# Kernel optimization log

Hardware: AMD Instinct MI355X
Metric: run time of the kernel (lower is better)

Reference implementation:

```python
import jax, jax.numpy as jnp
import numpy as np

B, K, N = 8, 4, 131072
T = B * K * N  # upper bound on packed length
NEG_IDLE = -1e8   # logit value forced when slot is idle
NEG_FILL = -1000.0  # padded-output fill value for logits


def setup_inputs() -> dict:
    key = jax.random.key(0)
    k1, k2, k3, k4, k5, k6 = jax.random.split(key, 6)
    return {
        "rgb": jax.random.normal(k1, (T, 3), dtype=jnp.float32),
        "logits_surface": jax.random.normal(k2, (T, 1), dtype=jnp.float32),
        "logits_air": jax.random.normal(k3, (T, 1), dtype=jnp.float32),
        "mask_surface": jax.random.bernoulli(k4, 0.5, (B, K, N)),
        "mask_air": jax.random.bernoulli(k5, 0.5, (B, K, N)),
        "idle_states": jax.random.uniform(k6, (B, K), dtype=jnp.float32),
    }


def reference(rgb, logits_surface, logits_air, mask_surface, mask_air, idle_states):
    # Packed arrays are laid out in flattened (b, k, n) order: the packed index of a
    # masked element equals the count of True entries preceding it -> cumsum - 1.
    Bb, Kk, Nn = mask_surface.shape
    scale = (1.0 - idle_states)[:, :, None, None]          # [B,K,1,1]
    idle = idle_states[:, :, None, None]                   # [B,K,1,1]

    ms_flat = mask_surface.reshape(-1)
    idx_s = (jnp.cumsum(ms_flat.astype(jnp.int32)) - 1).reshape(Bb, Kk, Nn)
    ms = mask_surface[..., None]                           # [B,K,N,1]

    rgb_g = jnp.take(rgb, idx_s, axis=0)                   # [B,K,N,3]
    rgb_out = jnp.where(ms, rgb_g * scale, 0.0)

    ls_g = jnp.take(logits_surface, idx_s, axis=0)         # [B,K,N,1]
    logits_surface_out = jnp.where(ms, ls_g * scale + idle * NEG_IDLE, NEG_FILL)

    ma_flat = mask_air.reshape(-1)
    idx_a = (jnp.cumsum(ma_flat.astype(jnp.int32)) - 1).reshape(Bb, Kk, Nn)
    ma = mask_air[..., None]
    la_g = jnp.take(logits_air, idx_a, axis=0)             # [B,K,N,1]
    logits_air_out = jnp.where(ma, la_g * scale + idle * NEG_IDLE, NEG_FILL)

    return rgb_out, logits_surface_out, logits_air_out
```

## Files before the change

### kernel.cpp

```cpp
#include <hip/hip_runtime.h>
#include <stdint.h>

#define T_TOTAL  4194304
#define NEG_IDLE (-100000000.0f)
#define NEG_FILL (-1000.0f)

#define BLOCK   256
#define EPT     8
#define EPB     (BLOCK * EPT)
#define NBLOCKS (T_TOTAL / EPB)


__device__ __forceinline__ unsigned decode8_i32(const uint4* p) {
    const uint4 a = p[0], b = p[1];
    return (a.x ? 1u : 0u) | (a.y ? 2u : 0u) | (a.z ? 4u : 0u) | (a.w ? 8u : 0u)
         | (b.x ? 16u : 0u) | (b.y ? 32u : 0u) | (b.z ? 64u : 0u) | (b.w ? 128u : 0u);
}

__global__ __launch_bounds__(BLOCK) void reduce_pack_kernel(
    const uint4* __restrict__ ms,
    const uint4* __restrict__ ma,
    unsigned long long* __restrict__ sums,
    unsigned short* __restrict__ packed)
{
    const int blk  = blockIdx.x;
    const int tid  = threadIdx.x;
    const int lane = tid & 63;
    const int wave = tid >> 6;
    const size_t e = (size_t)blk * EPB + (size_t)tid * EPT;

    const unsigned bits_s = decode8_i32(ms + (e >> 2));
    const unsigned bits_a = decode8_i32(ma + (e >> 2));
    packed[blk * BLOCK + tid] = (unsigned short)(bits_s | (bits_a << 8));

    unsigned long long v =
        ((unsigned long long)(unsigned)__popc(bits_a) << 32) | (unsigned)__popc(bits_s);
    #pragma unroll
    for (int d = 32; d; d >>= 1) v += __shfl_down(v, d, 64);

    __shared__ unsigned long long w[BLOCK / 64];
    if (lane == 0) w[wave] = v;
    __syncthreads();
    if (tid == 0) sums[blk] = w[0] + w[1] + w[2] + w[3];
}

__global__ __launch_bounds__(BLOCK) void scatter_kernel(
    const float* __restrict__ rgb,
    const float* __restrict__ ls,
    const float* __restrict__ la,
    const unsigned long long* __restrict__ sums,
    const unsigned short* __restrict__ packed,
    const float* __restrict__ idle_states,
    float* __restrict__ out)
{
    const int blk  = blockIdx.x;
    const int tid  = threadIdx.x;
    const int lane = tid & 63;
    const int wave = tid >> 6;
    const size_t base = (size_t)blk * EPB + (size_t)tid * EPT;

    const unsigned p = packed[blk * BLOCK + tid];
    const unsigned bits_s = p & 0xffu;
    const unsigned bits_a = p >> 8;

    unsigned long long acc = 0;
    {
        const ulonglong2* s2 = (const ulonglong2*)sums;
        const int i0 = tid * 8;
        #pragma unroll
        for (int q = 0; q < 4; ++q) {
            const ulonglong2 v = s2[tid * 4 + q];
            const int i = i0 + 2 * q;
            acc += (i     < blk) ? v.x : 0ull;
            acc += (i + 1 < blk) ? v.y : 0ull;
        }
        #pragma unroll
        for (int d = 32; d; d >>= 1) acc += __shfl_down(acc, d, 64);
    }

    const unsigned long long pk =
        ((unsigned long long)(unsigned)__popc(bits_a) << 32) | (unsigned)__popc(bits_s);
    unsigned long long incl = pk;
    #pragma unroll
    for (int d = 1; d < 64; d <<= 1) {
        unsigned long long t = __shfl_up(incl, d, 64);
        if (lane >= d) incl += t;
    }
    unsigned long long excl = incl - pk;

    __shared__ unsigned long long wtot[BLOCK / 64];
    __shared__ unsigned long long wpre[BLOCK / 64];
    if (lane == 63) wtot[wave] = incl;
    if (lane == 0)  wpre[wave] = acc;
    __syncthreads();
    #pragma unroll
    for (int w = 0; w < BLOCK / 64; ++w)
        if (w < wave) excl += wtot[w];
    const unsigned long long pre = wpre[0] + wpre[1] + wpre[2] + wpre[3];

    const int idx_s0 = (int)((pre + excl) & 0xffffffffULL);
    const int idx_a0 = (int)((pre + excl) >> 32);

    int is_[EPT], ia_[EPT];
    #pragma unroll
    for (int j = 0; j < EPT; ++j) {
        is_[j] = idx_s0 + __popc(bits_s & ((1u << j) - 1u));
        ia_[j] = idx_a0 + __popc(bits_a & ((1u << j) - 1u));
    }

    float r[3 * EPT], sv[EPT], av[EPT];
    #pragma unroll
    for (int j = 0; j < EPT; ++j) {
        const float* rp = rgb + (size_t)is_[j] * 3;
        r[3 * j + 0] = rp[0];
        r[3 * j + 1] = rp[1];
        r[3 * j + 2] = rp[2];
        sv[j] = ls[is_[j]];
        av[j] = la[ia_[j]];
    }

    const float idle      = idle_states[blk >> 6];
    const float scale     = 1.0f - idle;
    const float idle_term = idle * NEG_IDLE;
    #pragma unroll
    for (int j = 0; j < EPT; ++j) {
        const bool bs = (bits_s >> j) & 1u;
        const bool ba = (bits_a >> j) & 1u;
        r[3 * j + 0] = bs ? r[3 * j + 0] * scale : 0.0f;
        r[3 * j + 1] = bs ? r[3 * j + 1] * scale : 0.0f;
        r[3 * j + 2] = bs ? r[3 * j + 2] * scale : 0.0f;
        sv[j] = bs ? (sv[j] * scale + idle_term) : NEG_FILL;
        av[j] = ba ? (av[j] * scale + idle_term) : NEG_FILL;
    }

    float4* prgb = (float4*)(out + base * 3);
    #pragma unroll
    for (int j = 0; j < 6; ++j) prgb[j] = ((const float4*)r)[j];

    float4* pls = (float4*)(out + (size_t)3 * T_TOTAL + base);
    pls[0] = ((const float4*)sv)[0];
    pls[1] = ((const float4*)sv)[1];

    float4* pla = (float4*)(out + (size_t)4 * T_TOTAL + base);
    pla[0] = ((const float4*)av)[0];
    pla[1] = ((const float4*)av)[1];
}

extern "C" void kernel_launch(void* const* d_in, const int* in_sizes, int n_in,
                              void* d_out, int out_size, void* d_ws, size_t ws_size,
                              hipStream_t stream) {
    const float* rgb  = (const float*)d_in[0];
    const float* ls   = (const float*)d_in[1];
    const float* la   = (const float*)d_in[2];
    const uint4* ms   = (const uint4*)d_in[3];
    const uint4* ma   = (const uint4*)d_in[4];
    const float* idle = (const float*)d_in[5];
    float* out = (float*)d_out;

    unsigned long long* sums   = (unsigned long long*)d_ws;
    unsigned short*     packed = (unsigned short*)((uint8_t*)d_ws + NBLOCKS * sizeof(unsigned long long));

    reduce_pack_kernel<<<NBLOCKS, BLOCK, 0, stream>>>(ms, ma, sums, packed);
    scatter_kernel<<<NBLOCKS, BLOCK, 0, stream>>>(rgb, ls, la, sums, packed,
                                                  idle, out);
}
```

Baseline: 185.3 us.

## Split scatter kernel into three output roles and use nontemporal loads/stores

Measured after the change: 232.0 us. 1.25x slower.

```diff
diff --git a/kernel.cpp b/kernel.cpp
--- a/kernel.cpp
+++ b/kernel.cpp
@@ -5,21 +5,25 @@
 #define NEG_IDLE (-100000000.0f)
 #define NEG_FILL (-1000.0f)
 
-#define BLOCK   256
-#define EPT     8
-#define EPB     (BLOCK * EPT)
-#define NBLOCKS (T_TOTAL / EPB)
+#define BLOCK  256
+#define EPT    8
+#define EPB    (BLOCK * EPT)
+#define NCHUNK (T_TOTAL / EPB)
 
 
-__device__ __forceinline__ unsigned decode8_i32(const uint4* p) {
-    const uint4 a = p[0], b = p[1];
+typedef float    f32x4 __attribute__((ext_vector_type(4)));
+typedef unsigned u32x4 __attribute__((ext_vector_type(4)));
+
+__device__ __forceinline__ unsigned decode8_i32(const u32x4* p) {
+    const u32x4 a = __builtin_nontemporal_load(p);
+    const u32x4 b = __builtin_nontemporal_load(p + 1);
     return (a.x ? 1u : 0u) | (a.y ? 2u : 0u) | (a.z ? 4u : 0u) | (a.w ? 8u : 0u)
          | (b.x ? 16u : 0u) | (b.y ? 32u : 0u) | (b.z ? 64u : 0u) | (b.w ? 128u : 0u);
 }
 
 __global__ __launch_bounds__(BLOCK) void reduce_pack_kernel(
-    const uint4* __restrict__ ms,
-    const uint4* __restrict__ ma,
+    const u32x4* __restrict__ ms,
+    const u32x4* __restrict__ ma,
     unsigned long long* __restrict__ sums,
     unsigned short* __restrict__ packed)
 {
@@ -53,15 +57,17 @@
     const float* __restrict__ idle_states,
     float* __restrict__ out)
 {
-    const int blk  = blockIdx.x;
+    const int bid  = blockIdx.x;
+    const int role = bid >> 11;
+    const int blk  = bid & (NCHUNK - 1);
     const int tid  = threadIdx.x;
     const int lane = tid & 63;
     const int wave = tid >> 6;
     const size_t base = (size_t)blk * EPB + (size_t)tid * EPT;
 
-    const unsigned p = packed[blk * BLOCK + tid];
-    const unsigned bits_s = p & 0xffu;
-    const unsigned bits_a = p >> 8;
+    const unsigned pw   = packed[blk * BLOCK + tid];
+    const unsigned bits = (role == 2) ? (pw >> 8) : (pw & 0xffu);
+    const int c = __popc(bits);
 
     unsigned long long acc = 0;
     {
@@ -78,17 +84,15 @@
         for (int d = 32; d; d >>= 1) acc += __shfl_down(acc, d, 64);
     }
 
-    const unsigned long long pk =
-        ((unsigned long long)(unsigned)__popc(bits_a) << 32) | (unsigned)__popc(bits_s);
-    unsigned long long incl = pk;
+    int incl = c;
     #pragma unroll
     for (int d = 1; d < 64; d <<= 1) {
-        unsigned long long t = __shfl_up(incl, d, 64);
+        const int t = __shfl_up(incl, d, 64);
         if (lane >= d) incl += t;
     }
-    unsigned long long excl = incl - pk;
+    int excl = incl - c;
 
-    __shared__ unsigned long long wtot[BLOCK / 64];
+    __shared__ int wtot[BLOCK / 64];
     __shared__ unsigned long long wpre[BLOCK / 64];
     if (lane == 63) wtot[wave] = incl;
     if (lane == 0)  wpre[wave] = acc;
@@ -97,53 +101,56 @@
     for (int w = 0; w < BLOCK / 64; ++w)
         if (w < wave) excl += wtot[w];
     const unsigned long long pre = wpre[0] + wpre[1] + wpre[2] + wpre[3];
+    const int pre32 = (role == 2) ? (int)(pre >> 32) : (int)(pre & 0xffffffffull);
+    const int idx0  = pre32 + excl;
 
-    const int idx_s0 = (int)((pre + excl) & 0xffffffffULL);
-    const int idx_a0 = (int)((pre + excl) >> 32);
-
-    int is_[EPT], ia_[EPT];
+    int idx[EPT];
     #pragma unroll
-    for (int j = 0; j < EPT; ++j) {
-        is_[j] = idx_s0 + __popc(bits_s & ((1u << j) - 1u));
-        ia_[j] = idx_a0 + __popc(bits_a & ((1u << j) - 1u));
-    }
-
-    float r[3 * EPT], sv[EPT], av[EPT];
-    #pragma unroll
-    for (int j = 0; j < EPT; ++j) {
-        const float* rp = rgb + (size_t)is_[j] * 3;
-        r[3 * j + 0] = rp[0];
-        r[3 * j + 1] = rp[1];
-        r[3 * j + 2] = rp[2];
-        sv[j] = ls[is_[j]];
-        av[j] = la[ia_[j]];
-    }
+    for (int j = 0; j < EPT; ++j)
+        idx[j] = idx0 + __popc(bits & ((1u << j) - 1u));
 
     const float idle      = idle_states[blk >> 6];
     const float scale     = 1.0f - idle;
     const float idle_term = idle * NEG_IDLE;
-    #pragma unroll
-    for (int j = 0; j < EPT; ++j) {
-        const bool bs = (bits_s >> j) & 1u;
-        const bool ba = (bits_a >> j) & 1u;
-        r[3 * j + 0] = bs ? r[3 * j + 0] * scale : 0.0f;
-        r[3 * j + 1] = bs ? r[3 * j + 1] * scale : 0.0f;
-        r[3 * j + 2] = bs ? r[3 * j + 2] * scale : 0.0f;
-        sv[j] = bs ? (sv[j] * scale + idle_term) : NEG_FILL;
-        av[j] = ba ? (av[j] * scale + idle_term) : NEG_FILL;
+
+    if (role == 0) {
+        float r[3 * EPT];
+        #pragma unroll
+        for (int j = 0; j < EPT; ++j) {
+            const float* rp = rgb + (size_t)idx[j] * 3;
+            r[3 * j + 0] = rp[0];
+            r[3 * j + 1] = rp[1];
+            r[3 * j + 2] = rp[2];
+        }
+        #pragma unroll
+        for (int j = 0; j < EPT; ++j) {
+            const bool bs = (bits >> j) & 1u;
+            r[3 * j + 0] = bs ? r[3 * j + 0] * scale : 0.0f;
+            r[3 * j + 1] = bs ? r[3 * j + 1] * scale : 0.0f;
+            r[3 * j + 2] = bs ? r[3 * j + 2] * scale : 0.0f;
+        }
+        f32x4* dst = (f32x4*)(out + base * 3);
+        #pragma unroll
+        for (int j = 0; j < 6; ++j) {
+            const f32x4 v = { r[4 * j + 0], r[4 * j + 1], r[4 * j + 2], r[4 * j + 3] };
+            __builtin_nontemporal_store(v, dst + j);
+        }
+    } else {
+        const float* src = (role == 1) ? ls : la;
+        float v[EPT];
+        #pragma unroll
+        for (int j = 0; j < EPT; ++j) v[j] = src[idx[j]];
+        #pragma unroll
+        for (int j = 0; j < EPT; ++j) {
+            const bool b = (bits >> j) & 1u;
+            v[j] = b ? (v[j] * scale + idle_term) : NEG_FILL;
+        }
+        float* obase = out + (size_t)(2 + role) * T_TOTAL + base;
+        const f32x4 v0 = { v[0], v[1], v[2], v[3] };
+        const f32x4 v1 = { v[4], v[5], v[6], v[7] };
+        __builtin_nontemporal_store(v0, (f32x4*)obase);
+        __builtin_nontemporal_store(v1, (f32x4*)obase + 1);
     }
-
-    float4* prgb = (float4*)(out + base * 3);
-    #pragma unroll
-    for (int j = 0; j < 6; ++j) prgb[j] = ((const float4*)r)[j];
-
-    float4* pls = (float4*)(out + (size_t)3 * T_TOTAL + base);
-    pls[0] = ((const float4*)sv)[0];
-    pls[1] = ((const float4*)sv)[1];
-
-    float4* pla = (float4*)(out + (size_t)4 * T_TOTAL + base);
-    pla[0] = ((const float4*)av)[0];
-    pla[1] = ((const float4*)av)[1];
 }
 
 extern "C" void kernel_launch(void* const* d_in, const int* in_sizes, int n_in,
@@ -152,15 +159,16 @@
     const float* rgb  = (const float*)d_in[0];
     const float* ls   = (const float*)d_in[1];
     const float* la   = (const float*)d_in[2];
-    const uint4* ms   = (const uint4*)d_in[3];
-    const uint4* ma   = (const uint4*)d_in[4];
+    const u32x4* ms   = (const u32x4*)d_in[3];
+    const u32x4* ma   = (const u32x4*)d_in[4];
     const float* idle = (const float*)d_in[5];
     float* out = (float*)d_out;
 
     unsigned long long* sums   = (unsigned long long*)d_ws;
-    unsigned short*     packed = (unsigned short*)((uint8_t*)d_ws + NBLOCKS * sizeof(unsigned long long));
+    unsigned short*     packed =
+        (unsigned short*)((uint8_t*)d_ws + NCHUNK * sizeof(unsigned long long));
 
-    reduce_pack_kernel<<<NBLOCKS, BLOCK, 0, stream>>>(ms, ma, sums, packed);
-    scatter_kernel<<<NBLOCKS, BLOCK, 0, stream>>>(rgb, ls, la, sums, packed,
-                                                  idle, out);
+    reduce_pack_kernel<<<NCHUNK, BLOCK, 0, stream>>>(ms, ma, sums, packed);
+    scatter_kernel<<<3 * NCHUNK, BLOCK, 0, stream>>>(rgb, ls, la, sums, packed,
+                                                     idle, out);
 }
```
